# Kernel tuning notes

Hardware: AMD Instinct MI355X
Metric: run time of the kernel (lower is better)

The kernel has to match this reference:

```python
import jax, jax.numpy as jnp
import numpy as np

D = 512          # input_size (feature dim)
C = 100          # num_classes
N = 2048         # test samples
ALPHA = 0.5      # regularization mixing parameter
SHRINK = 1e-4    # shrinkage_param


def setup_inputs() -> dict:
    key = jax.random.key(0)
    k1, k2, k3, k4, k5 = jax.random.split(key, 5)
    X = jax.random.normal(k1, (N, D), dtype=jnp.float32)
    muK = jax.random.normal(k2, (C, D), dtype=jnp.float32)
    # Per-class covariances: PSD, well-conditioned (like fitted streaming covariances)
    A = jax.random.normal(k3, (C, D, D), dtype=jnp.float32) * 0.05
    SigmaK = jnp.einsum('cij,ckj->cik', A, A) + 0.1 * jnp.eye(D, dtype=jnp.float32)
    B = jax.random.normal(k4, (D, D), dtype=jnp.float32) * 0.05
    Sigma = B @ B.T + 0.1 * jnp.eye(D, dtype=jnp.float32)
    # class counts (all > 0 so every class is active)
    cK = jax.random.uniform(k5, (C,), dtype=jnp.float32, minval=1.0, maxval=1000.0)
    return {"X": X, "muK": muK, "SigmaK": SigmaK, "Sigma": Sigma, "cK": cK}


def reference(X, muK, SigmaK, Sigma, cK):
    # RegSigmaK[k] = alpha * SigmaK[k] + (1-alpha) * Sigma           [C, D, D]
    RegSigmaK = ALPHA * SigmaK + (1.0 - ALPHA) * Sigma[None, :, :]
    # priors (classes with zero count get prior 1, then are masked to -inf below)
    s = jnp.sum(cK)
    prior = jnp.where(cK == 0, 1.0, cK / s)                          # [C]
    # Lambda[k] = pinv((1-sh) * RegSigmaK[k] + sh * I)               [C, D, D]
    eye = jnp.eye(D, dtype=RegSigmaK.dtype)
    Lambda = jnp.linalg.pinv((1.0 - SHRINK) * RegSigmaK + SHRINK * eye)
    # 0.5 * log ||RegSigmaK[k]||_F  (torch.norm default = Frobenius)
    half_lognorm = 0.5 * jnp.log(jnp.linalg.norm(RegSigmaK, axis=(1, 2)))  # [C]
    # batched Mahalanobis quadratic form: (x - mu_k)^T Lambda_k (x - mu_k)
    diff = X[:, None, :] - muK[None, :, :]                           # [N, C, D]
    quad = jnp.einsum('ncd,cde,nce->nc', diff, Lambda, diff)         # [N, C]
    scores = jnp.log(prior)[None, :] - half_lognorm[None, :] - 0.5 * quad
    scores = jnp.where((cK == 0)[None, :], -jnp.inf, scores)
    return scores
```

## Files before the change

kernel.cpp:

```cpp
#include <hip/hip_runtime.h>
#include <math.h>

#define DIM 512
#define NCLS 100
#define NS 2048
#define DD (DIM*DIM)
#define SHRINKV 1e-4f

typedef short bf16x8 __attribute__((ext_vector_type(8)));
typedef short s16x4 __attribute__((ext_vector_type(4)));
typedef float f32x4 __attribute__((ext_vector_type(4)));

static __device__ __forceinline__ short f2bf(float f) {
  unsigned int u = __float_as_uint(f);
  u += 0x7FFFu + ((u >> 16) & 1u);
  return (short)(u >> 16);
}

static __device__ __forceinline__ int xcd_swz(int bid, int nwg) {
  int xcd = bid & 7, idx = bid >> 3;
  int q = nwg >> 3, r = nwg & 7;
  return (xcd < r ? xcd * (q + 1) : r * (q + 1) + (xcd - r) * q) + idx;
}

__global__ __launch_bounds__(256) void prep_kernel(const float* __restrict__ SigmaK,
                                                   const float* __restrict__ Sigma,
                                                   float* __restrict__ M,
                                                   float* __restrict__ aux) {
  int b = blockIdx.x;
  int k = b >> 2, chunk = b & 3;
  const float* Sk = SigmaK + (size_t)k * DD;
  float* Mk = M + (size_t)k * DD;
  int base0 = chunk << 16;
  float fro = 0.f;
  const float oms = 1.0f - SHRINKV;
  for (int it = 0; it < 64; ++it) {
    int idx = base0 + (it << 10) + (threadIdx.x << 2);
    float4 a = *(const float4*)(Sk + idx);
    float4 g = *(const float4*)(Sigma + idx);
    int r = idx >> 9, c = idx & 511;
    float4 reg;
    reg.x = 0.5f*(a.x + g.x); reg.y = 0.5f*(a.y + g.y);
    reg.z = 0.5f*(a.z + g.z); reg.w = 0.5f*(a.w + g.w);
    fro += reg.x*reg.x + reg.y*reg.y + reg.z*reg.z + reg.w*reg.w;
    float4 m;
    m.x = oms*reg.x + ((r == c + 0) ? SHRINKV : 0.f);
    m.y = oms*reg.y + ((r == c + 1) ? SHRINKV : 0.f);
    m.z = oms*reg.z + ((r == c + 2) ? SHRINKV : 0.f);
    m.w = oms*reg.w + ((r == c + 3) ? SHRINKV : 0.f);
    *(float4*)(Mk + idx) = m;
  }
  __shared__ float red[4];
  int lane = threadIdx.x & 63, w = threadIdx.x >> 6;
  for (int o = 32; o > 0; o >>= 1) fro += __shfl_down(fro, o);
  if (lane == 0) red[w] = fro;
  __syncthreads();
  if (threadIdx.x == 0) atomicAdd(&aux[1 + k], red[0] + red[1] + red[2] + red[3]);
}

static __device__ __forceinline__ void fdiag_dev(float* __restrict__ Mk,
                                                 short* __restrict__ Wk,
                                                 int p0, int lane,
                                                 float* __restrict__ Llds) {
  float row[64];
  const float* src = Mk + (size_t)(p0 + lane) * DIM + p0;
  #pragma unroll
  for (int c4 = 0; c4 < 64; c4 += 4) {
    float4 v = *(const float4*)(src + c4);
    row[c4] = v.x; row[c4+1] = v.y; row[c4+2] = v.z; row[c4+3] = v.w;
  }
  #pragma unroll
  for (int j = 0; j < 64; ++j) {
    float diagv = __shfl(row[j], j);
    float dv = sqrtf(diagv);
    float rinv = 1.0f / dv;
    float myLj = row[j] * rinv;
    row[j] = myLj;
    #pragma unroll
    for (int c = j + 1; c < 64; ++c)
      row[c] = fmaf(-myLj, __shfl(myLj, c), row[c]);
  }
  #pragma unroll
  for (int c = 0; c < 64; ++c)
    Llds[lane * 68 + c] = (c <= lane) ? row[c] : 0.f;
  float w[64];
  #pragma unroll
  for (int r = 0; r < 64; ++r) {
    float s = 0.f;
    #pragma unroll
    for (int kk = 0; kk + 4 <= r; kk += 4) {
      float4 lv = *(const float4*)(Llds + r*68 + kk);
      s += lv.x*w[kk] + lv.y*w[kk+1] + lv.z*w[kk+2] + lv.w*w[kk+3];
    }
    #pragma unroll
    for (int kk = r & ~3; kk < r; ++kk) s += Llds[r*68 + kk] * w[kk];
    float rhs = ((r == lane) ? 1.0f : 0.0f) - s;
    w[r] = rhs / Llds[r*68 + r];
  }
  #pragma unroll
  for (int r = 0; r < 64; ++r) {
    Mk[(size_t)(p0 + r)*DIM + p0 + lane] = w[r];
    Wk[(size_t)(p0 + r)*DIM + p0 + lane] = f2bf(w[r]);
  }
}

__global__ __launch_bounds__(64) void fdiag_kernel(float* __restrict__ M,
                                                   short* __restrict__ Wb) {
  __shared__ float Llds[64 * 68];
  fdiag_dev(M + (size_t)blockIdx.x * DD, Wb + (size_t)blockIdx.x * DD,
            0, threadIdx.x, Llds);
}

__global__ __launch_bounds__(256) void panelA_kernel(float* __restrict__ M,
                                                     short* __restrict__ Wb, int p) {
  __shared__ float SA[2][64 * 68];
  __shared__ float SB[2][64 * 68];
  int n = 7 - p;
  int nwg = n + p;
  int wg = xcd_swz(blockIdx.x, NCLS * nwg);
  int cls = wg / nwg, r = wg % nwg;
  float* Mk = M + (size_t)cls * DD;
  short* Wk = Wb + (size_t)cls * DD;
  int tid = threadIdx.x;
  int ty = tid >> 4, tx = tid & 15;
  int sr = tid >> 2, sq = (tid & 3) << 4;
  int p0 = p << 6;

  if (r < n) {
    int i = p + 1 + r;
    {
      const float* a = Mk + (size_t)((i << 6) + sr)*DIM + p0 + sq;
      const float* b = Mk + (size_t)(p0 + sr)*DIM + p0 + sq;
      #pragma unroll
      for (int t4 = 0; t4 < 4; ++t4) {
        float4 va = *(const float4*)(a + 4*t4);
        SA[0][(sq+4*t4+0)*68+sr]=va.x; SA[0][(sq+4*t4+1)*68+sr]=va.y;
        SA[0][(sq+4*t4+2)*68+sr]=va.z; SA[0][(sq+4*t4+3)*68+sr]=va.w;
        float4 vb = *(const float4*)(b + 4*t4);
        SA[1][(sq+4*t4+0)*68+sr]=vb.x; SA[1][(sq+4*t4+1)*68+sr]=vb.y;
        SA[1][(sq+4*t4+2)*68+sr]=vb.z; SA[1][(sq+4*t4+3)*68+sr]=vb.w;
      }
    }
    __syncthreads();
    float acc[4][4];
    #pragma unroll
    for (int a2 = 0; a2 < 4; ++a2)
      #pragma unroll
      for (int b2 = 0; b2 < 4; ++b2) acc[a2][b2] = 0.f;
    #pragma unroll 16
    for (int m = 0; m < 64; ++m) {
      float4 av = *(const float4*)(&SA[0][m*68 + (ty << 2)]);
      float4 bv = *(const float4*)(&SA[1][m*68 + (tx << 2)]);
      float a4[4] = {av.x, av.y, av.z, av.w};
      float b4[4] = {bv.x, bv.y, bv.z, bv.w};
      #pragma unroll
      for (int ir = 0; ir < 4; ++ir)
        #pragma unroll
        for (int ic = 0; ic < 4; ++ic) acc[ir][ic] += a4[ir] * b4[ic];
    }
    #pragma unroll
    for (int q = 0; q < 4; ++q) {
      float4 v; v.x = acc[q][0]; v.y = acc[q][1]; v.z = acc[q][2]; v.w = acc[q][3];
      *(float4*)(Mk + (size_t)((i << 6) + (ty << 2) + q)*DIM + p0 + (tx << 2)) = v;
    }
    if (r == 0) {
      __syncthreads();
      #pragma unroll
      for (int q = 0; q < 4; ++q)
        #pragma unroll
        for (int cc = 0; cc < 4; ++cc)
          SA[0][((tx << 2) + cc)*68 + (ty << 2) + q] = acc[q][cc];
      __syncthreads();
      float s2[4][4];
      #pragma unroll
      for (int a2 = 0; a2 < 4; ++a2)
        #pragma unroll
        for (int b2 = 0; b2 < 4; ++b2) s2[a2][b2] = 0.f;
      #pragma unroll 16
      for (int m = 0; m < 64; ++m) {
        float4 av = *(const float4*)(&SA[0][m*68 + (ty << 2)]);
        float4 bv = *(const float4*)(&SA[0][m*68 + (tx << 2)]);
        float a4[4] = {av.x, av.y, av.z, av.w};
        float b4[4] = {bv.x, bv.y, bv.z, bv.w};
        #pragma unroll
        for (int ir = 0; ir < 4; ++ir)
          #pragma unroll
          for (int ic = 0; ic < 4; ++ic) s2[ir][ic] += a4[ir] * b4[ic];
      }
      int d0 = (p + 1) << 6;
      #pragma unroll
      for (int q = 0; q < 4; ++q) {
        float* dst = Mk + (size_t)(d0 + (ty << 2) + q)*DIM + d0 + (tx << 2);
        float4 v = *(const float4*)dst;
        v.x -= s2[q][0]; v.y -= s2[q][1]; v.z -= s2[q][2]; v.w -= s2[q][3];
        *(float4*)dst = v;
      }
      __syncthreads();
      if (tid < 64)
        fdiag_dev(Mk, Wk, d0, tid, SA[1]);
    }
  } else {
    int j = r - n;
    auto stageLW = [&](int k, int buf) {
      const float* a = Mk + (size_t)(p0 + sr)*DIM + (k << 6) + sq;
      const float* b = Mk + (size_t)((j << 6) + sr)*DIM + (k << 6) + sq;
      #pragma unroll
      for (int t4 = 0; t4 < 4; ++t4) {
        float4 va = *(const float4*)(a + 4*t4);
        SA[buf][(sq+4*t4+0)*68+sr]=va.x; SA[buf][(sq+4*t4+1)*68+sr]=va.y;
        SA[buf][(sq+4*t4+2)*68+sr]=va.z; SA[buf][(sq+4*t4+3)*68+sr]=va.w;
        *(float4*)(&SB[buf][sr*68 + sq + 4*t4]) = *(const float4*)(b + 4*t4);
      }
    };
    float acc[4][4];
    #pragma unroll
    for (int a = 0; a < 4; ++a)
      #pragma unroll
      for (int b = 0; b < 4; ++b) acc[a][b] = 0.f;
    stageLW(j, 0);
    __syncthreads();
    int cur = 0;
    for (int k = j; k < p; ++k) {
      if (k + 1 < p) stageLW(k + 1, cur ^ 1);
      #pragma unroll 16
      for (int m = 0; m < 64; ++m) {
        float4 av = *(const float4*)(&SA[cur][m*68 + (ty << 2)]);
        float4 bv = *(const float4*)(&SB[cur][m*68 + (tx << 2)]);
        float a4[4] = {av.x, av.y, av.z, av.w};
        float b4[4] = {bv.x, bv.y, bv.z, bv.w};
        #pragma unroll
        for (int ir = 0; ir < 4; ++ir)
          #pragma unroll
          for (int ic = 0; ic < 4; ++ic) acc[ir][ic] += a4[ir] * b4[ic];
      }
      __syncthreads();
      cur ^= 1;
    }
    #pragma unroll
    for (int q = 0; q < 4; ++q) {
      float4 v; v.x = acc[q][0]; v.y = acc[q][1]; v.z = acc[q][2]; v.w = acc[q][3];
      *(float4*)(&SB[0][((ty << 2) + q)*68 + (tx << 2)]) = v;
    }
    {
      const float* a = Mk + (size_t)(p0 + sr)*DIM + p0 + sq;
      #pragma unroll
      for (int t4 = 0; t4 < 4; ++t4) {
        float4 va = *(const float4*)(a + 4*t4);
        SA[0][(sq+4*t4+0)*68+sr]=va.x; SA[0][(sq+4*t4+1)*68+sr]=va.y;
        SA[0][(sq+4*t4+2)*68+sr]=va.z; SA[0][(sq+4*t4+3)*68+sr]=va.w;
      }
    }
    __syncthreads();
    float r2[4][4];
    #pragma unroll
    for (int a = 0; a < 4; ++a)
      #pragma unroll
      for (int b = 0; b < 4; ++b) r2[a][b] = 0.f;
    #pragma unroll 16
    for (int m = 0; m < 64; ++m) {
      float4 av = *(const float4*)(&SA[0][m*68 + (ty << 2)]);
      float4 bv = *(const float4*)(&SB[0][m*68 + (tx << 2)]);
      float a4[4] = {av.x, av.y, av.z, av.w};
      float b4[4] = {bv.x, bv.y, bv.z, bv.w};
      #pragma unroll
      for (int ir = 0; ir < 4; ++ir)
        #pragma unroll
        for (int ic = 0; ic < 4; ++ic) r2[ir][ic] += a4[ir] * b4[ic];
    }
    #pragma unroll
    for (int q = 0; q < 4; ++q) {
      int a = (ty << 2) + q;
      float4 v; v.x = -r2[q][0]; v.y = -r2[q][1]; v.z = -r2[q][2]; v.w = -r2[q][3];
      *(float4*)(Mk + (size_t)((j << 6) + a)*DIM + p0 + (tx << 2)) = v;
      s16x4 h;
      h[0] = f2bf(v.x); h[1] = f2bf(v.y); h[2] = f2bf(v.z); h[3] = f2bf(v.w);
      *(s16x4*)(Wk + (size_t)(p0 + a)*DIM + (j << 6) + (tx << 2)) = h;
    }
  }
}

__global__ __launch_bounds__(256) void panelB_kernel(float* __restrict__ M, int p) {
  __shared__ float TA[64 * 68];
  __shared__ float TB[64 * 68];
  int n = 7 - p;
  int T = n * (n + 1) / 2;
  int nwg = NCLS * (T - 1);
  int wg = xcd_swz(blockIdx.x, nwg);
  int cls = wg / (T - 1);
  int t = wg % (T - 1) + 1;
  int bi = 0;
  while (t > bi) { t -= bi + 1; ++bi; }
  int i = p + 1 + bi, j = p + 1 + t;
  float* Mk = M + (size_t)cls * DD;
  int tid = threadIdx.x;
  int ty = tid >> 4, tx = tid & 15;
  int sr = tid >> 2, sq = (tid & 3) << 4;
  {
    const float* a = Mk + (size_t)((i << 6) + sr)*DIM + (p << 6) + sq;
    const float* b = Mk + (size_t)((j << 6) + sr)*DIM + (p << 6) + sq;
    #pragma unroll
    for (int t4 = 0; t4 < 4; ++t4) {
      float4 va = *(const float4*)(a + 4*t4);
      TA[(sq+4*t4+0)*68+sr]=va.x; TA[(sq+4*t4+1)*68+sr]=va.y;
      TA[(sq+4*t4+2)*68+sr]=va.z; TA[(sq+4*t4+3)*68+sr]=va.w;
      float4 vb = *(const float4*)(b + 4*t4);
      TB[(sq+4*t4+0)*68+sr]=vb.x; TB[(sq+4*t4+1)*68+sr]=vb.y;
      TB[(sq+4*t4+2)*68+sr]=vb.z; TB[(sq+4*t4+3)*68+sr]=vb.w;
    }
  }
  __syncthreads();
  float acc[4][4];
  #pragma unroll
  for (int a = 0; a < 4; ++a)
    #pragma unroll
    for (int b = 0; b < 4; ++b) acc[a][b] = 0.f;
  #pragma unroll 16
  for (int m = 0; m < 64; ++m) {
    float4 av = *(const float4*)(TA + m*68 + (ty << 2));
    float4 bv = *(const float4*)(TB + m*68 + (tx << 2));
    float a4[4] = {av.x, av.y, av.z, av.w};
    float b4[4] = {bv.x, bv.y, bv.z, bv.w};
    #pragma unroll
    for (int ir = 0; ir < 4; ++ir)
      #pragma unroll
      for (int ic = 0; ic < 4; ++ic) acc[ir][ic] += a4[ir] * b4[ic];
  }
  #pragma unroll
  for (int q = 0; q < 4; ++q) {
    float* dst = Mk + (size_t)((i << 6) + (ty << 2) + q)*DIM + (j << 6) + (tx << 2);
    float4 v = *(const float4*)dst;
    v.x -= acc[q][0]; v.y -= acc[q][1]; v.z -= acc[q][2]; v.w -= acc[q][3];
    *(float4*)dst = v;
  }
}

__global__ __launch_bounds__(256) void score_kernel(const float* __restrict__ X,
                                                    const float* __restrict__ muK,
                                                    const float* __restrict__ cK,
                                                    const short* __restrict__ W,
                                                    const float* __restrict__ aux,
                                                    float* __restrict__ out) {
  __shared__ __align__(16) char WB4[4][8192];
  __shared__ float sred[4];
  int bid = blockIdx.x;
  int wg = ((bid & 7) * 400) + (bid >> 3);
  int kc = wg >> 5;
  int n0 = (wg & 31) << 6;
  int tid = threadIdx.x;
  int lane = tid & 63, wv = tid >> 6;
  const short* Wk = W + (size_t)kc * DD;
  const float* mu = muK + (size_t)kc * DIM;
  int r16 = lane & 15;
  int k8 = (lane >> 4) << 3;
  int arow = (wv << 4) + r16;

  int lrow = lane >> 3;
  int lcolel = ((lane & 7) ^ lrow) << 3;

  constexpr int SJT[36] = {0,1,1, 2,3,2,3,2,3,3, 4,5,4,5,4,5,4,5,4,5,5,
                           6,7,6,7,6,7,6,7,6,7,6,7,6,7,7};
  constexpr int SDC[36] = {0,0,1, 0,0,1,1,2,2,3, 0,0,1,1,2,2,3,3,4,4,5,
                           0,0,1,1,2,2,3,3,4,4,5,5,6,6,7};

  bf16x8 af[8][2];
  #pragma unroll
  for (int dc = 0; dc < 8; ++dc) {
    #pragma unroll
    for (int ks = 0; ks < 2; ++ks) {
      int col = (dc << 6) + (ks << 5) + k8;
      const float* xp = X + (size_t)(n0 + arow)*DIM + col;
      float4 x0 = *(const float4*)xp;
      float4 x1 = *(const float4*)(xp + 4);
      float4 m0 = *(const float4*)(mu + col);
      float4 m1 = *(const float4*)(mu + col + 4);
      bf16x8 h;
      h[0]=f2bf(x0.x-m0.x); h[1]=f2bf(x0.y-m0.y); h[2]=f2bf(x0.z-m0.z); h[3]=f2bf(x0.w-m0.w);
      h[4]=f2bf(x1.x-m1.x); h[5]=f2bf(x1.y-m1.y); h[6]=f2bf(x1.z-m1.z); h[7]=f2bf(x1.w-m1.w);
      af[dc][ks] = h;
    }
  }

  auto issue = [&](int s) {
    const int b = s & 3;
    const int rbase = SJT[s] << 6;
    const int cc = (SDC[s] << 6) + lcolel;
    #pragma unroll
    for (int q = 0; q < 2; ++q) {
      const short* g = Wk + (size_t)(rbase + (q << 5) + (wv << 3) + lrow)*DIM + cc;
      __builtin_amdgcn_global_load_lds(
          (const __attribute__((address_space(1))) void*)g,
          (__attribute__((address_space(3))) void*)(WB4[b] + (q << 12) + (wv << 10)),
          16, 0, 0);
    }
  };

  float qp[4] = {0.f, 0.f, 0.f, 0.f};
  f32x4 acc[2][4];
  #pragma unroll
  for (int a = 0; a < 2; ++a)
    #pragma unroll
    for (int jj = 0; jj < 4; ++jj) { acc[a][jj][0]=0.f; acc[a][jj][1]=0.f; acc[a][jj][2]=0.f; acc[a][jj][3]=0.f; }

  issue(0);
  issue(1);
  #pragma unroll
  for (int s = 0; s < 36; ++s) {
    const int jt = SJT[s], dc = SDC[s];
    if (s + 2 < 36) issue(s + 2);
    if (s < 34)      asm volatile("s_waitcnt vmcnt(4)" ::: "memory");
    else if (s == 34) asm volatile("s_waitcnt vmcnt(2)" ::: "memory");
    else              asm volatile("s_waitcnt vmcnt(0)" ::: "memory");
    __builtin_amdgcn_s_barrier();
    __builtin_amdgcn_sched_barrier(0);
    __builtin_amdgcn_s_setprio(1);
    #pragma unroll
    for (int ks = 0; ks < 2; ++ks) {
      #pragma unroll
      for (int jj = 0; jj < 4; ++jj) {
        int brow = (jj << 4) + r16;
        bf16x8 bfr = *(const bf16x8*)((const char*)WB4[s & 3] +
                     (((brow << 7) + (((ks << 5) + k8) << 1)) ^ ((brow & 7) << 4)));
        acc[jt & 1][jj] = __builtin_amdgcn_mfma_f32_16x16x32_bf16(af[dc][ks], bfr, acc[jt & 1][jj], 0, 0, 0);
      }
    }
    __builtin_amdgcn_s_setprio(0);
    if (s == 2 || s == 9 || s == 20 || s == 35) {
      #pragma unroll
      for (int a = 0; a < 2; ++a)
        #pragma unroll
        for (int jj = 0; jj < 4; ++jj)
          #pragma unroll
          for (int r = 0; r < 4; ++r) {
            float y = acc[a][jj][r]; qp[r] += y * y;
            acc[a][jj][r] = 0.f;
          }
    }
  }
  #pragma unroll
  for (int r = 0; r < 4; ++r) {
    qp[r] += __shfl_xor(qp[r], 1);
    qp[r] += __shfl_xor(qp[r], 2);
    qp[r] += __shfl_xor(qp[r], 4);
    qp[r] += __shfl_xor(qp[r], 8);
  }
  {
    float v = (tid < NCLS) ? cK[tid] : 0.f;
    #pragma unroll
    for (int o = 32; o > 0; o >>= 1) v += __shfl_xor(v, o);
    if (lane == 0) sred[wv] = v;
  }
  __syncthreads();
  float sumck = sred[0] + sred[1] + sred[2] + sred[3];
  float ck = cK[kc];
  float base;
  if (ck == 0.f) base = -INFINITY;
  else base = logf(ck) - logf(sumck) - 0.25f * logf(aux[1 + kc]);
  if ((lane & 15) == 0) {
    int nbase = n0 + (wv << 4) + ((lane >> 4) << 2);
    #pragma unroll
    for (int r = 0; r < 4; ++r)
      out[(size_t)(nbase + r)*NCLS + kc] = base - 0.5f * qp[r];
  }
}

extern "C" void kernel_launch(void* const* d_in, const int* in_sizes, int n_in,
                              void* d_out, int out_size, void* d_ws, size_t ws_size,
                              hipStream_t stream) {
  (void)in_sizes; (void)n_in; (void)out_size; (void)ws_size;
  const float* X      = (const float*)d_in[0];
  const float* muK    = (const float*)d_in[1];
  const float* SigmaK = (const float*)d_in[2];
  const float* Sigma  = (const float*)d_in[3];
  const float* cK     = (const float*)d_in[4];
  float* out = (float*)d_out;
  char* ws = (char*)d_ws;
  float* M   = (float*)ws;
  short* W   = (short*)(ws + (size_t)NCLS * DD * 4);
  float* aux = (float*)(ws + (size_t)NCLS * DD * 6);

  (void)hipMemsetAsync(aux, 0, (1 + NCLS) * sizeof(float), stream);
  prep_kernel<<<400, 256, 0, stream>>>(SigmaK, Sigma, M, aux);
  fdiag_kernel<<<NCLS, 64, 0, stream>>>(M, W);
  for (int p = 0; p < 8; ++p) {
    int n = 7 - p;
    int nwg = n + p;
    panelA_kernel<<<NCLS * nwg, 256, 0, stream>>>(M, W, p);
    int Tm1 = n * (n + 1) / 2 - 1;
    if (Tm1 > 0) panelB_kernel<<<NCLS * Tm1, 256, 0, stream>>>(M, p);
  }
  score_kernel<<<NCLS * 32, 256, 0, stream>>>(X, muK, cK, W, aux, out);
}
```

Baseline: 827.6 us.

## Switch blocked Cholesky update from right-looking to left-looking, merging panel kernels

Replaces the right-looking trailing update (panelA plus panelB launches per step) with a left-looking scheme. Each panel block now accumulates contributions from all previous panels itself using a double-buffered LDS loop, and the lead block also builds the next diagonal update. This halves the kernel launches per step and drops the separate trailing-update pass with its read-modify-write traffic. In exchange, per-block work grows with p, and the fixed grid of 7 blocks per class leaves some blocks idle.

Result: slower. 911.1 us (+10.1%).

```diff
diff --git a/kernel.cpp b/kernel.cpp
--- a/kernel.cpp
+++ b/kernel.cpp
@@ -111,14 +111,13 @@
             0, threadIdx.x, Llds);
 }
 
-__global__ __launch_bounds__(256) void panelA_kernel(float* __restrict__ M,
+__global__ __launch_bounds__(256) void panelL_kernel(float* __restrict__ M,
                                                      short* __restrict__ Wb, int p) {
   __shared__ float SA[2][64 * 68];
   __shared__ float SB[2][64 * 68];
+  int wg = xcd_swz(blockIdx.x, NCLS * 7);
+  int cls = wg / 7, r = wg % 7;
   int n = 7 - p;
-  int nwg = n + p;
-  int wg = xcd_swz(blockIdx.x, NCLS * nwg);
-  int cls = wg / nwg, r = wg % nwg;
   float* Mk = M + (size_t)cls * DD;
   short* Wk = Wb + (size_t)cls * DD;
   int tid = threadIdx.x;
@@ -127,55 +126,104 @@
   int p0 = p << 6;
 
   if (r < n) {
-    int i = p + 1 + r;
-    {
-      const float* a = Mk + (size_t)((i << 6) + sr)*DIM + p0 + sq;
-      const float* b = Mk + (size_t)(p0 + sr)*DIM + p0 + sq;
+    const int i = p + 1 + r;
+    const bool lead = (r == 0);
+    float acc[4][4], s2[4][4];
+    #pragma unroll
+    for (int a2 = 0; a2 < 4; ++a2)
+      #pragma unroll
+      for (int b2 = 0; b2 < 4; ++b2) { acc[a2][b2] = 0.f; s2[a2][b2] = 0.f; }
+    auto stage2T = [&](int q, int buf) {
+      const float* a = Mk + (size_t)((i << 6) + sr)*DIM + (q << 6) + sq;
+      const float* b = Mk + (size_t)(p0 + sr)*DIM + (q << 6) + sq;
       #pragma unroll
       for (int t4 = 0; t4 < 4; ++t4) {
         float4 va = *(const float4*)(a + 4*t4);
-        SA[0][(sq+4*t4+0)*68+sr]=va.x; SA[0][(sq+4*t4+1)*68+sr]=va.y;
-        SA[0][(sq+4*t4+2)*68+sr]=va.z; SA[0][(sq+4*t4+3)*68+sr]=va.w;
+        SA[buf][(sq+4*t4+0)*68+sr]=va.x; SA[buf][(sq+4*t4+1)*68+sr]=va.y;
+        SA[buf][(sq+4*t4+2)*68+sr]=va.z; SA[buf][(sq+4*t4+3)*68+sr]=va.w;
         float4 vb = *(const float4*)(b + 4*t4);
-        SA[1][(sq+4*t4+0)*68+sr]=vb.x; SA[1][(sq+4*t4+1)*68+sr]=vb.y;
-        SA[1][(sq+4*t4+2)*68+sr]=vb.z; SA[1][(sq+4*t4+3)*68+sr]=vb.w;
+        SB[buf][(sq+4*t4+0)*68+sr]=vb.x; SB[buf][(sq+4*t4+1)*68+sr]=vb.y;
+        SB[buf][(sq+4*t4+2)*68+sr]=vb.z; SB[buf][(sq+4*t4+3)*68+sr]=vb.w;
+      }
+    };
+    if (p > 0) {
+      stage2T(0, 0);
+      __syncthreads();
+      int cur = 0;
+      for (int q = 0; q < p; ++q) {
+        if (q + 1 < p) stage2T(q + 1, cur ^ 1);
+        #pragma unroll 16
+        for (int m = 0; m < 64; ++m) {
+          float4 av = *(const float4*)(&SA[cur][m*68 + (ty << 2)]);
+          float4 bv = *(const float4*)(&SB[cur][m*68 + (tx << 2)]);
+          float a4[4] = {av.x, av.y, av.z, av.w};
+          float b4[4] = {bv.x, bv.y, bv.z, bv.w};
+          #pragma unroll
+          for (int ir = 0; ir < 4; ++ir)
+            #pragma unroll
+            for (int ic = 0; ic < 4; ++ic) acc[ir][ic] += a4[ir] * b4[ic];
+          if (lead) {
+            float4 cv = *(const float4*)(&SA[cur][m*68 + (tx << 2)]);
+            float c4[4] = {cv.x, cv.y, cv.z, cv.w};
+            #pragma unroll
+            for (int ir = 0; ir < 4; ++ir)
+              #pragma unroll
+              for (int ic = 0; ic < 4; ++ic) s2[ir][ic] += a4[ir] * c4[ic];
+          }
+        }
+        __syncthreads();
+        cur ^= 1;
+      }
+    }
+    #pragma unroll
+    for (int q4 = 0; q4 < 4; ++q4) {
+      float4 v = *(const float4*)(Mk + (size_t)((i << 6) + (ty << 2) + q4)*DIM + p0 + (tx << 2));
+      float d0v = v.x - acc[q4][0], d1 = v.y - acc[q4][1];
+      float d2 = v.z - acc[q4][2], d3 = v.w - acc[q4][3];
+      SA[0][((tx << 2) + 0)*68 + (ty << 2) + q4] = d0v;
+      SA[0][((tx << 2) + 1)*68 + (ty << 2) + q4] = d1;
+      SA[0][((tx << 2) + 2)*68 + (ty << 2) + q4] = d2;
+      SA[0][((tx << 2) + 3)*68 + (ty << 2) + q4] = d3;
+    }
+    {
+      const float* b = Mk + (size_t)(p0 + sr)*DIM + p0 + sq;
+      #pragma unroll
+      for (int t4 = 0; t4 < 4; ++t4) {
+        float4 vb = *(const float4*)(b + 4*t4);
+        SB[0][(sq+4*t4+0)*68+sr]=vb.x; SB[0][(sq+4*t4+1)*68+sr]=vb.y;
+        SB[0][(sq+4*t4+2)*68+sr]=vb.z; SB[0][(sq+4*t4+3)*68+sr]=vb.w;
       }
     }
     __syncthreads();
-    float acc[4][4];
+    float l2[4][4];
     #pragma unroll
     for (int a2 = 0; a2 < 4; ++a2)
       #pragma unroll
-      for (int b2 = 0; b2 < 4; ++b2) acc[a2][b2] = 0.f;
+      for (int b2 = 0; b2 < 4; ++b2) l2[a2][b2] = 0.f;
     #pragma unroll 16
     for (int m = 0; m < 64; ++m) {
       float4 av = *(const float4*)(&SA[0][m*68 + (ty << 2)]);
-      float4 bv = *(const float4*)(&SA[1][m*68 + (tx << 2)]);
+      float4 bv = *(const float4*)(&SB[0][m*68 + (tx << 2)]);
       float a4[4] = {av.x, av.y, av.z, av.w};
       float b4[4] = {bv.x, bv.y, bv.z, bv.w};
       #pragma unroll
       for (int ir = 0; ir < 4; ++ir)
         #pragma unroll
-        for (int ic = 0; ic < 4; ++ic) acc[ir][ic] += a4[ir] * b4[ic];
-    }
-    #pragma unroll
-    for (int q = 0; q < 4; ++q) {
-      float4 v; v.x = acc[q][0]; v.y = acc[q][1]; v.z = acc[q][2]; v.w = acc[q][3];
-      *(float4*)(Mk + (size_t)((i << 6) + (ty << 2) + q)*DIM + p0 + (tx << 2)) = v;
-    }
-    if (r == 0) {
+        for (int ic = 0; ic < 4; ++ic) l2[ir][ic] += a4[ir] * b4[ic];
+    }
+    #pragma unroll
+    for (int q4 = 0; q4 < 4; ++q4) {
+      float4 v; v.x = l2[q4][0]; v.y = l2[q4][1]; v.z = l2[q4][2]; v.w = l2[q4][3];
+      *(float4*)(Mk + (size_t)((i << 6) + (ty << 2) + q4)*DIM + p0 + (tx << 2)) = v;
+    }
+    if (lead) {
       __syncthreads();
       #pragma unroll
-      for (int q = 0; q < 4; ++q)
+      for (int q4 = 0; q4 < 4; ++q4)
         #pragma unroll
         for (int cc = 0; cc < 4; ++cc)
-          SA[0][((tx << 2) + cc)*68 + (ty << 2) + q] = acc[q][cc];
+          SA[0][((tx << 2) + cc)*68 + (ty << 2) + q4] = l2[q4][cc];
       __syncthreads();
-      float s2[4][4];
-      #pragma unroll
-      for (int a2 = 0; a2 < 4; ++a2)
-        #pragma unroll
-        for (int b2 = 0; b2 < 4; ++b2) s2[a2][b2] = 0.f;
       #pragma unroll 16
       for (int m = 0; m < 64; ++m) {
         float4 av = *(const float4*)(&SA[0][m*68 + (ty << 2)]);
@@ -187,12 +235,12 @@
           #pragma unroll
           for (int ic = 0; ic < 4; ++ic) s2[ir][ic] += a4[ir] * b4[ic];
       }
-      int d0 = (p + 1) << 6;
-      #pragma unroll
-      for (int q = 0; q < 4; ++q) {
-        float* dst = Mk + (size_t)(d0 + (ty << 2) + q)*DIM + d0 + (tx << 2);
+      const int d0 = (p + 1) << 6;
+      #pragma unroll
+      for (int q4 = 0; q4 < 4; ++q4) {
+        float* dst = Mk + (size_t)(d0 + (ty << 2) + q4)*DIM + d0 + (tx << 2);
         float4 v = *(const float4*)dst;
-        v.x -= s2[q][0]; v.y -= s2[q][1]; v.z -= s2[q][2]; v.w -= s2[q][3];
+        v.x -= s2[q4][0]; v.y -= s2[q4][1]; v.z -= s2[q4][2]; v.w -= s2[q4][3];
         *(float4*)dst = v;
       }
       __syncthreads();
@@ -276,61 +324,6 @@
       h[0] = f2bf(v.x); h[1] = f2bf(v.y); h[2] = f2bf(v.z); h[3] = f2bf(v.w);
       *(s16x4*)(Wk + (size_t)(p0 + a)*DIM + (j << 6) + (tx << 2)) = h;
     }
-  }
-}
-
-__global__ __launch_bounds__(256) void panelB_kernel(float* __restrict__ M, int p) {
-  __shared__ float TA[64 * 68];
-  __shared__ float TB[64 * 68];
-  int n = 7 - p;
-  int T = n * (n + 1) / 2;
-  int nwg = NCLS * (T - 1);
-  int wg = xcd_swz(blockIdx.x, nwg);
-  int cls = wg / (T - 1);
-  int t = wg % (T - 1) + 1;
-  int bi = 0;
-  while (t > bi) { t -= bi + 1; ++bi; }
-  int i = p + 1 + bi, j = p + 1 + t;
-  float* Mk = M + (size_t)cls * DD;
-  int tid = threadIdx.x;
-  int ty = tid >> 4, tx = tid & 15;
-  int sr = tid >> 2, sq = (tid & 3) << 4;
-  {
-    const float* a = Mk + (size_t)((i << 6) + sr)*DIM + (p << 6) + sq;
-    const float* b = Mk + (size_t)((j << 6) + sr)*DIM + (p << 6) + sq;
-    #pragma unroll
-    for (int t4 = 0; t4 < 4; ++t4) {
-      float4 va = *(const float4*)(a + 4*t4);
-      TA[(sq+4*t4+0)*68+sr]=va.x; TA[(sq+4*t4+1)*68+sr]=va.y;
-      TA[(sq+4*t4+2)*68+sr]=va.z; TA[(sq+4*t4+3)*68+sr]=va.w;
-      float4 vb = *(const float4*)(b + 4*t4);
-      TB[(sq+4*t4+0)*68+sr]=vb.x; TB[(sq+4*t4+1)*68+sr]=vb.y;
-      TB[(sq+4*t4+2)*68+sr]=vb.z; TB[(sq+4*t4+3)*68+sr]=vb.w;
-    }
-  }
-  __syncthreads();
-  float acc[4][4];
-  #pragma unroll
-  for (int a = 0; a < 4; ++a)
-    #pragma unroll
-    for (int b = 0; b < 4; ++b) acc[a][b] = 0.f;
-  #pragma unroll 16
-  for (int m = 0; m < 64; ++m) {
-    float4 av = *(const float4*)(TA + m*68 + (ty << 2));
-    float4 bv = *(const float4*)(TB + m*68 + (tx << 2));
-    float a4[4] = {av.x, av.y, av.z, av.w};
-    float b4[4] = {bv.x, bv.y, bv.z, bv.w};
-    #pragma unroll
-    for (int ir = 0; ir < 4; ++ir)
-      #pragma unroll
-      for (int ic = 0; ic < 4; ++ic) acc[ir][ic] += a4[ir] * b4[ic];
-  }
-  #pragma unroll
-  for (int q = 0; q < 4; ++q) {
-    float* dst = Mk + (size_t)((i << 6) + (ty << 2) + q)*DIM + (j << 6) + (tx << 2);
-    float4 v = *(const float4*)dst;
-    v.x -= acc[q][0]; v.y -= acc[q][1]; v.z -= acc[q][2]; v.w -= acc[q][3];
-    *(float4*)dst = v;
   }
 }
 
@@ -481,12 +474,7 @@
   (void)hipMemsetAsync(aux, 0, (1 + NCLS) * sizeof(float), stream);
   prep_kernel<<<400, 256, 0, stream>>>(SigmaK, Sigma, M, aux);
   fdiag_kernel<<<NCLS, 64, 0, stream>>>(M, W);
-  for (int p = 0; p < 8; ++p) {
-    int n = 7 - p;
-    int nwg = n + p;
-    panelA_kernel<<<NCLS * nwg, 256, 0, stream>>>(M, W, p);
-    int Tm1 = n * (n + 1) / 2 - 1;
-    if (Tm1 > 0) panelB_kernel<<<NCLS * Tm1, 256, 0, stream>>>(M, p);
-  }
+  for (int p = 0; p < 8; ++p)
+    panelL_kernel<<<NCLS * 7, 256, 0, stream>>>(M, W, p);
   score_kernel<<<NCLS * 32, 256, 0, stream>>>(X, muK, cK, W, aux, out);
 }
```

## Fuse blocked factorization launches into one persistent kernel with grid barriers

Applied to the files above, without the earlier changes.

Replaces the sequence of fdiag, panelA and panelB launches (about 16 kernels) with a single persistent kernel of 256 workgroups. The workgroups loop over the same tile work items and use an atomic-counter software grid barrier between phases. The diagonal factorization of the next block now runs as separate work items after the SYRK update instead of inside the r==0 panel workgroup. This removes launch gaps and tail effects, but adds barrier spin overhead, gives up the XCD swizzle, and relies on all 256 workgroups being co-resident.

Result: slower. 1.917 ms (+131.6%).

```diff
diff --git a/kernel.cpp b/kernel.cpp
--- a/kernel.cpp
+++ b/kernel.cpp
@@ -6,6 +6,7 @@
 #define NS 2048
 #define DD (DIM*DIM)
 #define SHRINKV 1e-4f
+#define FGRID 256
 
 typedef short bf16x8 __attribute__((ext_vector_type(8)));
 typedef short s16x4 __attribute__((ext_vector_type(4)));
@@ -17,10 +18,21 @@
   return (short)(u >> 16);
 }
 
-static __device__ __forceinline__ int xcd_swz(int bid, int nwg) {
-  int xcd = bid & 7, idx = bid >> 3;
-  int q = nwg >> 3, r = nwg & 7;
-  return (xcd < r ? xcd * (q + 1) : r * (q + 1) + (xcd - r) * q) + idx;
+static __device__ __forceinline__ void gsync(int* bar, int& ls) {
+  __syncthreads();
+  if (threadIdx.x == 0) {
+    ls ^= 1;
+    __threadfence();
+    if (atomicAdd(&bar[0], 1) == FGRID - 1) {
+      bar[0] = 0;
+      __threadfence();
+      atomicExch(&bar[1], ls);
+    } else {
+      while (atomicAdd(&bar[1], 0) != ls) __builtin_amdgcn_s_sleep(2);
+    }
+    __threadfence();
+  }
+  __syncthreads();
 }
 
 __global__ __launch_bounds__(256) void prep_kernel(const float* __restrict__ SigmaK,
@@ -104,233 +116,244 @@
   }
 }
 
-__global__ __launch_bounds__(64) void fdiag_kernel(float* __restrict__ M,
-                                                   short* __restrict__ Wb) {
-  __shared__ float Llds[64 * 68];
-  fdiag_dev(M + (size_t)blockIdx.x * DD, Wb + (size_t)blockIdx.x * DD,
-            0, threadIdx.x, Llds);
-}
-
-__global__ __launch_bounds__(256) void panelA_kernel(float* __restrict__ M,
-                                                     short* __restrict__ Wb, int p) {
+__global__ __launch_bounds__(256) void factor_kernel(float* __restrict__ M,
+                                                     short* __restrict__ Wb,
+                                                     int* __restrict__ bar) {
   __shared__ float SA[2][64 * 68];
   __shared__ float SB[2][64 * 68];
-  int n = 7 - p;
-  int nwg = n + p;
-  int wg = xcd_swz(blockIdx.x, NCLS * nwg);
-  int cls = wg / nwg, r = wg % nwg;
-  float* Mk = M + (size_t)cls * DD;
-  short* Wk = Wb + (size_t)cls * DD;
-  int tid = threadIdx.x;
-  int ty = tid >> 4, tx = tid & 15;
-  int sr = tid >> 2, sq = (tid & 3) << 4;
-  int p0 = p << 6;
-
-  if (r < n) {
-    int i = p + 1 + r;
-    {
-      const float* a = Mk + (size_t)((i << 6) + sr)*DIM + p0 + sq;
-      const float* b = Mk + (size_t)(p0 + sr)*DIM + p0 + sq;
-      #pragma unroll
-      for (int t4 = 0; t4 < 4; ++t4) {
-        float4 va = *(const float4*)(a + 4*t4);
-        SA[0][(sq+4*t4+0)*68+sr]=va.x; SA[0][(sq+4*t4+1)*68+sr]=va.y;
-        SA[0][(sq+4*t4+2)*68+sr]=va.z; SA[0][(sq+4*t4+3)*68+sr]=va.w;
-        float4 vb = *(const float4*)(b + 4*t4);
-        SA[1][(sq+4*t4+0)*68+sr]=vb.x; SA[1][(sq+4*t4+1)*68+sr]=vb.y;
-        SA[1][(sq+4*t4+2)*68+sr]=vb.z; SA[1][(sq+4*t4+3)*68+sr]=vb.w;
+  const int wgid = blockIdx.x;
+  const int tid = threadIdx.x;
+  const int ty = tid >> 4, tx = tid & 15;
+  const int sr = tid >> 2, sq = (tid & 3) << 4;
+  int ls = 0;
+
+  for (int w = wgid; w < NCLS; w += FGRID) {
+    __syncthreads();
+    if (tid < 64)
+      fdiag_dev(M + (size_t)w * DD, Wb + (size_t)w * DD, 0, tid, SA[0]);
+  }
+  __threadfence();
+  gsync(bar, ls);
+
+  for (int p = 0; p < 8; ++p) {
+    const int n = 7 - p;
+    const int p0 = p << 6;
+    for (int w = wgid; w < NCLS * 7; w += FGRID) {
+      int cls = w / 7, r = w % 7;
+      float* Mk = M + (size_t)cls * DD;
+      short* Wk = Wb + (size_t)cls * DD;
+      __syncthreads();
+      if (r < n) {
+        int i = p + 1 + r;
+        {
+          const float* a = Mk + (size_t)((i << 6) + sr)*DIM + p0 + sq;
+          const float* b = Mk + (size_t)(p0 + sr)*DIM + p0 + sq;
+          #pragma unroll
+          for (int t4 = 0; t4 < 4; ++t4) {
+            float4 va = *(const float4*)(a + 4*t4);
+            SA[0][(sq+4*t4+0)*68+sr]=va.x; SA[0][(sq+4*t4+1)*68+sr]=va.y;
+            SA[0][(sq+4*t4+2)*68+sr]=va.z; SA[0][(sq+4*t4+3)*68+sr]=va.w;
+            float4 vb = *(const float4*)(b + 4*t4);
+            SA[1][(sq+4*t4+0)*68+sr]=vb.x; SA[1][(sq+4*t4+1)*68+sr]=vb.y;
+            SA[1][(sq+4*t4+2)*68+sr]=vb.z; SA[1][(sq+4*t4+3)*68+sr]=vb.w;
+          }
+        }
+        __syncthreads();
+        float acc[4][4];
+        #pragma unroll
+        for (int a2 = 0; a2 < 4; ++a2)
+          #pragma unroll
+          for (int b2 = 0; b2 < 4; ++b2) acc[a2][b2] = 0.f;
+        #pragma unroll 16
+        for (int m = 0; m < 64; ++m) {
+          float4 av = *(const float4*)(&SA[0][m*68 + (ty << 2)]);
+          float4 bv = *(const float4*)(&SA[1][m*68 + (tx << 2)]);
+          float a4[4] = {av.x, av.y, av.z, av.w};
+          float b4[4] = {bv.x, bv.y, bv.z, bv.w};
+          #pragma unroll
+          for (int ir = 0; ir < 4; ++ir)
+            #pragma unroll
+            for (int ic = 0; ic < 4; ++ic) acc[ir][ic] += a4[ir] * b4[ic];
+        }
+        #pragma unroll
+        for (int q = 0; q < 4; ++q) {
+          float4 v; v.x = acc[q][0]; v.y = acc[q][1]; v.z = acc[q][2]; v.w = acc[q][3];
+          *(float4*)(Mk + (size_t)((i << 6) + (ty << 2) + q)*DIM + p0 + (tx << 2)) = v;
+        }
+        if (r == 0) {
+          __syncthreads();
+          #pragma unroll
+          for (int q = 0; q < 4; ++q)
+            #pragma unroll
+            for (int cc = 0; cc < 4; ++cc)
+              SA[0][((tx << 2) + cc)*68 + (ty << 2) + q] = acc[q][cc];
+          __syncthreads();
+          float s2[4][4];
+          #pragma unroll
+          for (int a2 = 0; a2 < 4; ++a2)
+            #pragma unroll
+            for (int b2 = 0; b2 < 4; ++b2) s2[a2][b2] = 0.f;
+          #pragma unroll 16
+          for (int m = 0; m < 64; ++m) {
+            float4 av = *(const float4*)(&SA[0][m*68 + (ty << 2)]);
+            float4 bv = *(const float4*)(&SA[0][m*68 + (tx << 2)]);
+            float a4[4] = {av.x, av.y, av.z, av.w};
+            float b4[4] = {bv.x, bv.y, bv.z, bv.w};
+            #pragma unroll
+            for (int ir = 0; ir < 4; ++ir)
+              #pragma unroll
+              for (int ic = 0; ic < 4; ++ic) s2[ir][ic] += a4[ir] * b4[ic];
+          }
+          int d0 = (p + 1) << 6;
+          #pragma unroll
+          for (int q = 0; q < 4; ++q) {
+            float* dst = Mk + (size_t)(d0 + (ty << 2) + q)*DIM + d0 + (tx << 2);
+            float4 v = *(const float4*)dst;
+            v.x -= s2[q][0]; v.y -= s2[q][1]; v.z -= s2[q][2]; v.w -= s2[q][3];
+            *(float4*)dst = v;
+          }
+        }
+      } else {
+        int j = r - n;
+        auto stageLW = [&](int k, int buf) {
+          const float* a = Mk + (size_t)(p0 + sr)*DIM + (k << 6) + sq;
+          const float* b = Mk + (size_t)((j << 6) + sr)*DIM + (k << 6) + sq;
+          #pragma unroll
+          for (int t4 = 0; t4 < 4; ++t4) {
+            float4 va = *(const float4*)(a + 4*t4);
+            SA[buf][(sq+4*t4+0)*68+sr]=va.x; SA[buf][(sq+4*t4+1)*68+sr]=va.y;
+            SA[buf][(sq+4*t4+2)*68+sr]=va.z; SA[buf][(sq+4*t4+3)*68+sr]=va.w;
+            *(float4*)(&SB[buf][sr*68 + sq + 4*t4]) = *(const float4*)(b + 4*t4);
+          }
+        };
+        float acc[4][4];
+        #pragma unroll
+        for (int a = 0; a < 4; ++a)
+          #pragma unroll
+          for (int b = 0; b < 4; ++b) acc[a][b] = 0.f;
+        stageLW(j, 0);
+        __syncthreads();
+        int cur = 0;
+        for (int k = j; k < p; ++k) {
+          if (k + 1 < p) stageLW(k + 1, cur ^ 1);
+          #pragma unroll 16
+          for (int m = 0; m < 64; ++m) {
+            float4 av = *(const float4*)(&SA[cur][m*68 + (ty << 2)]);
+            float4 bv = *(const float4*)(&SB[cur][m*68 + (tx << 2)]);
+            float a4[4] = {av.x, av.y, av.z, av.w};
+            float b4[4] = {bv.x, bv.y, bv.z, bv.w};
+            #pragma unroll
+            for (int ir = 0; ir < 4; ++ir)
+              #pragma unroll
+              for (int ic = 0; ic < 4; ++ic) acc[ir][ic] += a4[ir] * b4[ic];
+          }
+          __syncthreads();
+          cur ^= 1;
+        }
+        #pragma unroll
+        for (int q = 0; q < 4; ++q) {
+          float4 v; v.x = acc[q][0]; v.y = acc[q][1]; v.z = acc[q][2]; v.w = acc[q][3];
+          *(float4*)(&SB[0][((ty << 2) + q)*68 + (tx << 2)]) = v;
+        }
+        {
+          const float* a = Mk + (size_t)(p0 + sr)*DIM + p0 + sq;
+          #pragma unroll
+          for (int t4 = 0; t4 < 4; ++t4) {
+            float4 va = *(const float4*)(a + 4*t4);
+            SA[0][(sq+4*t4+0)*68+sr]=va.x; SA[0][(sq+4*t4+1)*68+sr]=va.y;
+            SA[0][(sq+4*t4+2)*68+sr]=va.z; SA[0][(sq+4*t4+3)*68+sr]=va.w;
+          }
+        }
+        __syncthreads();
+        float r2[4][4];
+        #pragma unroll
+        for (int a = 0; a < 4; ++a)
+          #pragma unroll
+          for (int b = 0; b < 4; ++b) r2[a][b] = 0.f;
+        #pragma unroll 16
+        for (int m = 0; m < 64; ++m) {
+          float4 av = *(const float4*)(&SA[0][m*68 + (ty << 2)]);
+          float4 bv = *(const float4*)(&SB[0][m*68 + (tx << 2)]);
+          float a4[4] = {av.x, av.y, av.z, av.w};
+          float b4[4] = {bv.x, bv.y, bv.z, bv.w};
+          #pragma unroll
+          for (int ir = 0; ir < 4; ++ir)
+            #pragma unroll
+            for (int ic = 0; ic < 4; ++ic) r2[ir][ic] += a4[ir] * b4[ic];
+        }
+        #pragma unroll
+        for (int q = 0; q < 4; ++q) {
+          int a = (ty << 2) + q;
+          float4 v; v.x = -r2[q][0]; v.y = -r2[q][1]; v.z = -r2[q][2]; v.w = -r2[q][3];
+          *(float4*)(Mk + (size_t)((j << 6) + a)*DIM + p0 + (tx << 2)) = v;
+          s16x4 h;
+          h[0] = f2bf(v.x); h[1] = f2bf(v.y); h[2] = f2bf(v.z); h[3] = f2bf(v.w);
+          *(s16x4*)(Wk + (size_t)(p0 + a)*DIM + (j << 6) + (tx << 2)) = h;
+        }
       }
     }
-    __syncthreads();
-    float acc[4][4];
-    #pragma unroll
-    for (int a2 = 0; a2 < 4; ++a2)
-      #pragma unroll
-      for (int b2 = 0; b2 < 4; ++b2) acc[a2][b2] = 0.f;
-    #pragma unroll 16
-    for (int m = 0; m < 64; ++m) {
-      float4 av = *(const float4*)(&SA[0][m*68 + (ty << 2)]);
-      float4 bv = *(const float4*)(&SA[1][m*68 + (tx << 2)]);
-      float a4[4] = {av.x, av.y, av.z, av.w};
-      float b4[4] = {bv.x, bv.y, bv.z, bv.w};
-      #pragma unroll
-      for (int ir = 0; ir < 4; ++ir)
-        #pragma unroll
-        for (int ic = 0; ic < 4; ++ic) acc[ir][ic] += a4[ir] * b4[ic];
-    }
-    #pragma unroll
-    for (int q = 0; q < 4; ++q) {
-      float4 v; v.x = acc[q][0]; v.y = acc[q][1]; v.z = acc[q][2]; v.w = acc[q][3];
-      *(float4*)(Mk + (size_t)((i << 6) + (ty << 2) + q)*DIM + p0 + (tx << 2)) = v;
-    }
-    if (r == 0) {
-      __syncthreads();
-      #pragma unroll
-      for (int q = 0; q < 4; ++q)
-        #pragma unroll
-        for (int cc = 0; cc < 4; ++cc)
-          SA[0][((tx << 2) + cc)*68 + (ty << 2) + q] = acc[q][cc];
-      __syncthreads();
-      float s2[4][4];
-      #pragma unroll
-      for (int a2 = 0; a2 < 4; ++a2)
-        #pragma unroll
-        for (int b2 = 0; b2 < 4; ++b2) s2[a2][b2] = 0.f;
-      #pragma unroll 16
-      for (int m = 0; m < 64; ++m) {
-        float4 av = *(const float4*)(&SA[0][m*68 + (ty << 2)]);
-        float4 bv = *(const float4*)(&SA[0][m*68 + (tx << 2)]);
-        float a4[4] = {av.x, av.y, av.z, av.w};
-        float b4[4] = {bv.x, bv.y, bv.z, bv.w};
-        #pragma unroll
-        for (int ir = 0; ir < 4; ++ir)
-          #pragma unroll
-          for (int ic = 0; ic < 4; ++ic) s2[ir][ic] += a4[ir] * b4[ic];
+    __threadfence();
+    gsync(bar, ls);
+    if (p < 7) {
+      const int T = n * (n + 1) / 2;
+      const int nsyrk = NCLS * (T - 1);
+      const int nB = nsyrk + NCLS;
+      for (int w = wgid; w < nB; w += FGRID) {
+        __syncthreads();
+        if (w >= nsyrk) {
+          int cls = w - nsyrk;
+          if (tid < 64)
+            fdiag_dev(M + (size_t)cls * DD, Wb + (size_t)cls * DD,
+                      (p + 1) << 6, tid, SA[0]);
+        } else {
+          int cls = w / (T - 1);
+          int t = w % (T - 1) + 1;
+          int bi = 0;
+          while (t > bi) { t -= bi + 1; ++bi; }
+          int i = p + 1 + bi, j = p + 1 + t;
+          float* Mk = M + (size_t)cls * DD;
+          {
+            const float* a = Mk + (size_t)((i << 6) + sr)*DIM + p0 + sq;
+            const float* b = Mk + (size_t)((j << 6) + sr)*DIM + p0 + sq;
+            #pragma unroll
+            for (int t4 = 0; t4 < 4; ++t4) {
+              float4 va = *(const float4*)(a + 4*t4);
+              SA[0][(sq+4*t4+0)*68+sr]=va.x; SA[0][(sq+4*t4+1)*68+sr]=va.y;
+              SA[0][(sq+4*t4+2)*68+sr]=va.z; SA[0][(sq+4*t4+3)*68+sr]=va.w;
+              float4 vb = *(const float4*)(b + 4*t4);
+              SA[1][(sq+4*t4+0)*68+sr]=vb.x; SA[1][(sq+4*t4+1)*68+sr]=vb.y;
+              SA[1][(sq+4*t4+2)*68+sr]=vb.z; SA[1][(sq+4*t4+3)*68+sr]=vb.w;
+            }
+          }
+          __syncthreads();
+          float acc[4][4];
+          #pragma unroll
+          for (int a2 = 0; a2 < 4; ++a2)
+            #pragma unroll
+            for (int b2 = 0; b2 < 4; ++b2) acc[a2][b2] = 0.f;
+          #pragma unroll 16
+          for (int m = 0; m < 64; ++m) {
+            float4 av = *(const float4*)(&SA[0][m*68 + (ty << 2)]);
+            float4 bv = *(const float4*)(&SA[1][m*68 + (tx << 2)]);
+            float a4[4] = {av.x, av.y, av.z, av.w};
+            float b4[4] = {bv.x, bv.y, bv.z, bv.w};
+            #pragma unroll
+            for (int ir = 0; ir < 4; ++ir)
+              #pragma unroll
+              for (int ic = 0; ic < 4; ++ic) acc[ir][ic] += a4[ir] * b4[ic];
+          }
+          #pragma unroll
+          for (int q = 0; q < 4; ++q) {
+            float* dst = Mk + (size_t)((i << 6) + (ty << 2) + q)*DIM + (j << 6) + (tx << 2);
+            float4 v = *(const float4*)dst;
+            v.x -= acc[q][0]; v.y -= acc[q][1]; v.z -= acc[q][2]; v.w -= acc[q][3];
+            *(float4*)dst = v;
+          }
+        }
       }
-      int d0 = (p + 1) << 6;
-      #pragma unroll
-      for (int q = 0; q < 4; ++q) {
-        float* dst = Mk + (size_t)(d0 + (ty << 2) + q)*DIM + d0 + (tx << 2);
-        float4 v = *(const float4*)dst;
-        v.x -= s2[q][0]; v.y -= s2[q][1]; v.z -= s2[q][2]; v.w -= s2[q][3];
-        *(float4*)dst = v;
-      }
-      __syncthreads();
-      if (tid < 64)
-        fdiag_dev(Mk, Wk, d0, tid, SA[1]);
-    }
-  } else {
-    int j = r - n;
-    auto stageLW = [&](int k, int buf) {
-      const float* a = Mk + (size_t)(p0 + sr)*DIM + (k << 6) + sq;
-      const float* b = Mk + (size_t)((j << 6) + sr)*DIM + (k << 6) + sq;
-      #pragma unroll
-      for (int t4 = 0; t4 < 4; ++t4) {
-        float4 va = *(const float4*)(a + 4*t4);
-        SA[buf][(sq+4*t4+0)*68+sr]=va.x; SA[buf][(sq+4*t4+1)*68+sr]=va.y;
-        SA[buf][(sq+4*t4+2)*68+sr]=va.z; SA[buf][(sq+4*t4+3)*68+sr]=va.w;
-        *(float4*)(&SB[buf][sr*68 + sq + 4*t4]) = *(const float4*)(b + 4*t4);
-      }
-    };
-    float acc[4][4];
-    #pragma unroll
-    for (int a = 0; a < 4; ++a)
-      #pragma unroll
-      for (int b = 0; b < 4; ++b) acc[a][b] = 0.f;
-    stageLW(j, 0);
-    __syncthreads();
-    int cur = 0;
-    for (int k = j; k < p; ++k) {
-      if (k + 1 < p) stageLW(k + 1, cur ^ 1);
-      #pragma unroll 16
-      for (int m = 0; m < 64; ++m) {
-        float4 av = *(const float4*)(&SA[cur][m*68 + (ty << 2)]);
-        float4 bv = *(const float4*)(&SB[cur][m*68 + (tx << 2)]);
-        float a4[4] = {av.x, av.y, av.z, av.w};
-        float b4[4] = {bv.x, bv.y, bv.z, bv.w};
-        #pragma unroll
-        for (int ir = 0; ir < 4; ++ir)
-          #pragma unroll
-          for (int ic = 0; ic < 4; ++ic) acc[ir][ic] += a4[ir] * b4[ic];
-      }
-      __syncthreads();
-      cur ^= 1;
-    }
-    #pragma unroll
-    for (int q = 0; q < 4; ++q) {
-      float4 v; v.x = acc[q][0]; v.y = acc[q][1]; v.z = acc[q][2]; v.w = acc[q][3];
-      *(float4*)(&SB[0][((ty << 2) + q)*68 + (tx << 2)]) = v;
-    }
-    {
-      const float* a = Mk + (size_t)(p0 + sr)*DIM + p0 + sq;
-      #pragma unroll
-      for (int t4 = 0; t4 < 4; ++t4) {
-        float4 va = *(const float4*)(a + 4*t4);
-        SA[0][(sq+4*t4+0)*68+sr]=va.x; SA[0][(sq+4*t4+1)*68+sr]=va.y;
-        SA[0][(sq+4*t4+2)*68+sr]=va.z; SA[0][(sq+4*t4+3)*68+sr]=va.w;
-      }
-    }
-    __syncthreads();
-    float r2[4][4];
-    #pragma unroll
-    for (int a = 0; a < 4; ++a)
-      #pragma unroll
-      for (int b = 0; b < 4; ++b) r2[a][b] = 0.f;
-    #pragma unroll 16
-    for (int m = 0; m < 64; ++m) {
-      float4 av = *(const float4*)(&SA[0][m*68 + (ty << 2)]);
-      float4 bv = *(const float4*)(&SB[0][m*68 + (tx << 2)]);
-      float a4[4] = {av.x, av.y, av.z, av.w};
-      float b4[4] = {bv.x, bv.y, bv.z, bv.w};
-      #pragma unroll
-      for (int ir = 0; ir < 4; ++ir)
-        #pragma unroll
-        for (int ic = 0; ic < 4; ++ic) r2[ir][ic] += a4[ir] * b4[ic];
-    }
-    #pragma unroll
-    for (int q = 0; q < 4; ++q) {
-      int a = (ty << 2) + q;
-      float4 v; v.x = -r2[q][0]; v.y = -r2[q][1]; v.z = -r2[q][2]; v.w = -r2[q][3];
-      *(float4*)(Mk + (size_t)((j << 6) + a)*DIM + p0 + (tx << 2)) = v;
-      s16x4 h;
-      h[0] = f2bf(v.x); h[1] = f2bf(v.y); h[2] = f2bf(v.z); h[3] = f2bf(v.w);
-      *(s16x4*)(Wk + (size_t)(p0 + a)*DIM + (j << 6) + (tx << 2)) = h;
-    }
-  }
-}
-
-__global__ __launch_bounds__(256) void panelB_kernel(float* __restrict__ M, int p) {
-  __shared__ float TA[64 * 68];
-  __shared__ float TB[64 * 68];
-  int n = 7 - p;
-  int T = n * (n + 1) / 2;
-  int nwg = NCLS * (T - 1);
-  int wg = xcd_swz(blockIdx.x, nwg);
-  int cls = wg / (T - 1);
-  int t = wg % (T - 1) + 1;
-  int bi = 0;
-  while (t > bi) { t -= bi + 1; ++bi; }
-  int i = p + 1 + bi, j = p + 1 + t;
-  float* Mk = M + (size_t)cls * DD;
-  int tid = threadIdx.x;
-  int ty = tid >> 4, tx = tid & 15;
-  int sr = tid >> 2, sq = (tid & 3) << 4;
-  {
-    const float* a = Mk + (size_t)((i << 6) + sr)*DIM + (p << 6) + sq;
-    const float* b = Mk + (size_t)((j << 6) + sr)*DIM + (p << 6) + sq;
-    #pragma unroll
-    for (int t4 = 0; t4 < 4; ++t4) {
-      float4 va = *(const float4*)(a + 4*t4);
-      TA[(sq+4*t4+0)*68+sr]=va.x; TA[(sq+4*t4+1)*68+sr]=va.y;
-      TA[(sq+4*t4+2)*68+sr]=va.z; TA[(sq+4*t4+3)*68+sr]=va.w;
-      float4 vb = *(const float4*)(b + 4*t4);
-      TB[(sq+4*t4+0)*68+sr]=vb.x; TB[(sq+4*t4+1)*68+sr]=vb.y;
-      TB[(sq+4*t4+2)*68+sr]=vb.z; TB[(sq+4*t4+3)*68+sr]=vb.w;
-    }
-  }
-  __syncthreads();
-  float acc[4][4];
-  #pragma unroll
-  for (int a = 0; a < 4; ++a)
-    #pragma unroll
-    for (int b = 0; b < 4; ++b) acc[a][b] = 0.f;
-  #pragma unroll 16
-  for (int m = 0; m < 64; ++m) {
-    float4 av = *(const float4*)(TA + m*68 + (ty << 2));
-    float4 bv = *(const float4*)(TB + m*68 + (tx << 2));
-    float a4[4] = {av.x, av.y, av.z, av.w};
-    float b4[4] = {bv.x, bv.y, bv.z, bv.w};
-    #pragma unroll
-    for (int ir = 0; ir < 4; ++ir)
-      #pragma unroll
-      for (int ic = 0; ic < 4; ++ic) acc[ir][ic] += a4[ir] * b4[ic];
-  }
-  #pragma unroll
-  for (int q = 0; q < 4; ++q) {
-    float* dst = Mk + (size_t)((i << 6) + (ty << 2) + q)*DIM + (j << 6) + (tx << 2);
-    float4 v = *(const float4*)dst;
-    v.x -= acc[q][0]; v.y -= acc[q][1]; v.z -= acc[q][2]; v.w -= acc[q][3];
-    *(float4*)dst = v;
+      __threadfence();
+      gsync(bar, ls);
+    }
   }
 }
 
@@ -477,16 +500,10 @@
   float* M   = (float*)ws;
   short* W   = (short*)(ws + (size_t)NCLS * DD * 4);
   float* aux = (float*)(ws + (size_t)NCLS * DD * 6);
-
-  (void)hipMemsetAsync(aux, 0, (1 + NCLS) * sizeof(float), stream);
+  int*   bar = (int*)(aux + 128);
+
+  (void)hipMemsetAsync(aux, 0, 132 * sizeof(float), stream);
   prep_kernel<<<400, 256, 0, stream>>>(SigmaK, Sigma, M, aux);
-  fdiag_kernel<<<NCLS, 64, 0, stream>>>(M, W);
-  for (int p = 0; p < 8; ++p) {
-    int n = 7 - p;
-    int nwg = n + p;
-    panelA_kernel<<<NCLS * nwg, 256, 0, stream>>>(M, W, p);
-    int Tm1 = n * (n + 1) / 2 - 1;
-    if (Tm1 > 0) panelB_kernel<<<NCLS * Tm1, 256, 0, stream>>>(M, p);
-  }
+  factor_kernel<<<FGRID, 256, 0, stream>>>(M, W, bar);
   score_kernel<<<NCLS * 32, 256, 0, stream>>>(X, muK, cK, W, aux, out);
 }
```
